# Kernel optimization log

Hardware: AMD Instinct MI355X
Metric: run time of the kernel (lower is better)

The kernel has to match this reference:

```python
import jax, jax.numpy as jnp
import numpy as np


def setup_inputs() -> dict:
    key = jax.random.key(0)
    ks = jax.random.split(key, 16)
    B, T, E, H, V = 64, 24, 512, 1024, 32000
    A = H  # attention_dim == hidden_size in original init
    s = 0.02  # init scale
    n = lambda k, shape: (jax.random.normal(k, shape, jnp.float32) * s)
    return {
        "features": jax.random.normal(ks[0], (B, E), jnp.float32),
        "captions": jax.random.randint(ks[1], (B, T), 0, V, dtype=jnp.int32),
        "lengths": jnp.full((B, 1), T + 1, dtype=jnp.int32),
        # learned parameters
        "emb": n(ks[2], (V, E)),
        "We": n(ks[3], (E, A)), "be": jnp.zeros((A,), jnp.float32),
        "Wd": n(ks[4], (H, A)), "bd": jnp.zeros((A,), jnp.float32),
        "va": n(ks[5], (A,)), "ba": jnp.zeros((), jnp.float32),
        "Wih": n(ks[6], (E, H)), "bih": jnp.zeros((H,), jnp.float32),
        "Wic": n(ks[7], (E, H)), "bic": jnp.zeros((H,), jnp.float32),
        "Wfb": n(ks[8], (H, E)), "bfb": jnp.zeros((E,), jnp.float32),
        "Wi": n(ks[9], (2 * E, 4 * H)), "Wh": n(ks[10], (H, 4 * H)),
        "bl": jnp.zeros((4 * H,), jnp.float32),
        "Wo": n(ks[11], (H, V)), "bo": jnp.zeros((V,), jnp.float32),
    }


def reference(features, captions, lengths, emb, We, be, Wd, bd, va, ba,
              Wih, bih, Wic, bic, Wfb, bfb, Wi, Wh, bl, Wo, bo):
    T = captions.shape[1]
    # embeddings = [features ; embed(captions)] -> [B, T+1, E]
    embeds = jnp.concatenate([features[:, None, :], emb[captions]], axis=1)
    mean_e = embeds.mean(axis=1)
    h = mean_e @ Wih + bih  # init_h
    c = mean_e @ Wic + bic  # init_c
    att1 = embeds @ We + be  # encoder projection, precomputed [B, L, A]

    def step(carry, emb_t):
        h, c = carry
        # additive attention over the full encoded sequence
        score = jnp.einsum('bla,a->bl', jax.nn.relu(att1 + (h @ Wd + bd)[:, None, :]), va) + ba
        alpha = jax.nn.softmax(score, axis=1)
        awe = jnp.einsum('bl,ble->be', alpha, embeds)
        gate = jax.nn.sigmoid(h @ Wfb + bfb)
        x = jnp.concatenate([emb_t, gate * awe], axis=-1)  # [B, 2E]
        z = x @ Wi + h @ Wh + bl
        i, f, g, o = jnp.split(z, 4, axis=-1)  # torch LSTM gate order i,f,g,o
        c = jax.nn.sigmoid(f) * c + jax.nn.sigmoid(i) * jnp.tanh(g)
        h = jax.nn.sigmoid(o) * jnp.tanh(c)
        return (h, c), h @ Wo + bo

    emb_seq = jnp.swapaxes(embeds[:, :T, :], 0, 1)  # [T, B, E]
    (_, _), logits = jax.lax.scan(step, (h, c), emb_seq)
    return jnp.swapaxes(logits, 0, 1)  # [B, T, V]
```

## Files before the change

### kernel.cpp

```cpp
#include <hip/hip_runtime.h>
#include <cstdio>
#include <cstdint>

#define B_ 64
#define T_ 24
#define L_ 25
#define E_ 512
#define H_ 1024
#define A_ 1024
#define V_ 32000
#define HCAT 5632

typedef unsigned short u16;
typedef short bf16x8 __attribute__((ext_vector_type(8)));
typedef float f32x4 __attribute__((ext_vector_type(4)));

__device__ __forceinline__ u16 f2bf(float f) {
    union { float f; unsigned int u; } v; v.f = f;
    unsigned int u = v.u;
    unsigned int r = (u + 0x7FFFu + ((u >> 16) & 1u)) >> 16;
    return (u16)r;
}
__device__ __forceinline__ float bf2f(u16 h) {
    union { unsigned int u; float f; } v; v.u = ((unsigned int)h) << 16;
    return v.f;
}
__device__ __forceinline__ void splitbf(float a, u16& hi, u16& lo) {
    hi = f2bf(a);
    lo = f2bf(a - bf2f(hi));
}
__device__ __forceinline__ float sigf(float x) { return 1.f / (1.f + __expf(-x)); }


__global__ void build_embeds(const float* __restrict__ features, const int* __restrict__ captions,
                             const float* __restrict__ emb, float* __restrict__ embeds,
                             float* __restrict__ mean_eT, u16* __restrict__ embsL2,
                             u16* __restrict__ embsA2) {
    int b = blockIdx.x; int e = threadIdx.x;
    float s = 0.f;
    for (int l = 0; l < L_; ++l) {
        float w;
        if (l == 0) w = features[b * E_ + e];
        else {
            int cap = captions[b * T_ + (l - 1)];
            w = emb[(size_t)cap * E_ + e];
        }
        embeds[(size_t)(b * L_ + l) * E_ + e] = w;
        s += w;
        u16 hi, lo; splitbf(w, hi, lo);
        size_t rl = (size_t)(b * L_ + l) * 1536;
        embsL2[rl + e] = hi; embsL2[rl + 512 + e] = lo; embsL2[rl + 1024 + e] = hi;
        if (l < T_) {
            size_t ra = (size_t)(l * 64 + b) * 1536;
            embsA2[ra + e] = hi; embsA2[ra + 512 + e] = lo; embsA2[ra + 1024 + e] = hi;
        }
    }
    mean_eT[e * B_ + b] = s * (1.f / 25.f);
}

__global__ void transpose_wo(const float* __restrict__ Wo, u16* __restrict__ WoT) {
    __shared__ float tile[32][33];
    int n0 = blockIdx.x * 32, k0 = blockIdx.y * 32;
    int tid = threadIdx.x;
    int tx = tid & 31, ty = tid >> 5;
    for (int i = ty; i < 32; i += 8)
        tile[i][tx] = Wo[(size_t)(k0 + i) * V_ + n0 + tx];
    __syncthreads();
    for (int i = ty; i < 32; i += 8)
        WoT[(size_t)(n0 + i) * H_ + k0 + tx] = f2bf(tile[tx][i]);
}

__global__ void tsplit(const float* __restrict__ W, u16* __restrict__ dst, int K, int srcld) {
    __shared__ float tile[32][33];
    int n0 = blockIdx.x * 32, k0 = blockIdx.y * 32;
    int tid = threadIdx.x;
    int tx = tid & 31, ty = tid >> 5;
    for (int i = ty; i < 32; i += 8)
        tile[i][tx] = W[(size_t)(k0 + i) * srcld + n0 + tx];
    __syncthreads();
    for (int i = ty; i < 32; i += 8) {
        float v = tile[tx][i];
        u16 hi, lo; splitbf(v, hi, lo);
        u16* d = dst + (size_t)(n0 + i) * (3 * K) + (k0 + tx);
        d[0] = hi; d[K] = hi; d[2 * K] = lo;
    }
}

__global__ void build_bcat(const float* __restrict__ bd, const float* __restrict__ bfb,
                           float* __restrict__ bcat) {
    int i = blockIdx.x * 256 + threadIdx.x;
    if (i < HCAT) bcat[i] = (i < 1024) ? bd[i] : ((i < 1536) ? bfb[i - 1024] : 0.f);
}

__global__ __launch_bounds__(1024) void init_hc(const float* __restrict__ mean_eT,
                                                const float* __restrict__ Wih, const float* __restrict__ bih,
                                                const float* __restrict__ Wic, const float* __restrict__ bic,
                                                u16* __restrict__ h2, float* __restrict__ c) {
    int tid = threadIdx.x; int ny = tid & 15, r = tid >> 4;
    int col = blockIdx.x * 16 + ny;
    int cc = (col < H_) ? col : col - H_;
    const float* Wp = (col < H_) ? Wih : Wic;
    const float* bp = (col < H_) ? bih : bic;
    float acc = bp[cc];
    for (int k = 0; k < E_; ++k) acc += mean_eT[k * B_ + r] * Wp[(size_t)k * H_ + cc];
    if (col < H_) {
        u16 hi, lo; splitbf(acc, hi, lo);
        h2[(size_t)r * 3072 + cc] = hi;
        h2[(size_t)r * 3072 + 1024 + cc] = lo;
        h2[(size_t)r * 3072 + 2048 + cc] = hi;
    } else c[r * H_ + cc] = acc;
}

template<int BM, int BN>
__global__ __launch_bounds__(256) void gemm_split(const u16* __restrict__ A2, const u16* __restrict__ B2T,
                                                  const float* __restrict__ bias, float* __restrict__ C,
                                                  int K3, int ldc) {
    constexpr int LDS = 40;
    __shared__ u16 As[BM * LDS];
    __shared__ u16 Bs[BN * LDS];
    constexpr int FM = BM / 32, FN = BN / 32;
    constexpr int ACH = BM / 64, BCH = BN / 64;
    int m0 = blockIdx.x * BM, n0 = blockIdx.y * BN;
    int tid = threadIdx.x, lane = tid & 63, wid = tid >> 6;
    int wm = wid >> 1, wn = wid & 1;

    f32x4 acc[FM][FN];
#pragma unroll
    for (int m = 0; m < FM; ++m)
#pragma unroll
        for (int n = 0; n < FN; ++n) acc[m][n] = (f32x4){0.f, 0.f, 0.f, 0.f};

    const u16* agp[ACH]; u16* asw[ACH];
    const u16* bgp[BCH]; u16* bsw[BCH];
#pragma unroll
    for (int i = 0; i < ACH; ++i) {
        int id = i * 256 + tid; int row = id >> 2, q = id & 3;
        agp[i] = A2 + (size_t)(m0 + row) * K3 + q * 8;
        asw[i] = As + row * LDS + q * 8;
    }
#pragma unroll
    for (int i = 0; i < BCH; ++i) {
        int id = i * 256 + tid; int row = id >> 2, q = id & 3;
        bgp[i] = B2T + (size_t)(n0 + row) * K3 + q * 8;
        bsw[i] = Bs + row * LDS + q * 8;
    }
    int rsel = lane & 15, kg = (lane >> 4) * 8;
    const u16* ard[FM]; const u16* brd[FN];
#pragma unroll
    for (int m = 0; m < FM; ++m) ard[m] = As + (wm * (BM / 2) + m * 16 + rsel) * LDS + kg;
#pragma unroll
    for (int n = 0; n < FN; ++n) brd[n] = Bs + (wn * (BN / 2) + n * 16 + rsel) * LDS + kg;

    uint4 ar[ACH], br[BCH];
#pragma unroll
    for (int i = 0; i < ACH; ++i) ar[i] = *(const uint4*)(agp[i]);
#pragma unroll
    for (int i = 0; i < BCH; ++i) br[i] = *(const uint4*)(bgp[i]);

    int nk = K3 / 32;
    for (int k = 0; k < nk; ++k) {
#pragma unroll
        for (int i = 0; i < ACH; ++i) *(uint4*)(asw[i]) = ar[i];
#pragma unroll
        for (int i = 0; i < BCH; ++i) *(uint4*)(bsw[i]) = br[i];
        __syncthreads();
        if (k + 1 < nk) {
            int kt = (k + 1) * 32;
#pragma unroll
            for (int i = 0; i < ACH; ++i) ar[i] = *(const uint4*)(agp[i] + kt);
#pragma unroll
            for (int i = 0; i < BCH; ++i) br[i] = *(const uint4*)(bgp[i] + kt);
        }
        bf16x8 aF[FM], bF[FN];
#pragma unroll
        for (int m = 0; m < FM; ++m) aF[m] = *(const bf16x8*)(ard[m]);
#pragma unroll
        for (int n = 0; n < FN; ++n) bF[n] = *(const bf16x8*)(brd[n]);
#pragma unroll
        for (int m = 0; m < FM; ++m)
#pragma unroll
            for (int n = 0; n < FN; ++n)
                acc[m][n] = __builtin_amdgcn_mfma_f32_16x16x32_bf16(aF[m], bF[n], acc[m][n], 0, 0, 0);
        __syncthreads();
    }

    int r4 = (lane >> 4) * 4, cn = lane & 15;
#pragma unroll
    for (int n = 0; n < FN; ++n) {
        int gcol = n0 + wn * (BN / 2) + n * 16 + cn;
        float bv = bias[gcol];
#pragma unroll
        for (int m = 0; m < FM; ++m) {
            int gr = m0 + wm * (BM / 2) + m * 16 + r4;
#pragma unroll
            for (int reg = 0; reg < 4; ++reg)
                C[(size_t)(gr + reg) * ldc + gcol] = acc[m][n][reg] + bv;
        }
    }
}


__global__ __launch_bounds__(256) void step_attn(const float* __restrict__ hcat, const float* __restrict__ att1,
                                                 const float* __restrict__ embeds, const float* __restrict__ va,
                                                 u16* __restrict__ x2s) {
    __shared__ float proj_s[1024], va_s[1024], sc_s[32], al_s[32];
    int b = blockIdx.x; int tid = threadIdx.x; int lane = tid & 63; int w = tid >> 6;
    for (int i = tid; i < 1024; i += 256) { proj_s[i] = hcat[b * HCAT + i]; va_s[i] = va[i]; }
    __syncthreads();
    for (int l = w; l < L_; l += 4) {
        const float* arow = att1 + (size_t)(b * L_ + l) * A_;
        float p = 0.f;
        for (int a = lane; a < A_; a += 64) {
            float v = arow[a] + proj_s[a];
            p += fmaxf(v, 0.f) * va_s[a];
        }
        for (int off = 32; off; off >>= 1) p += __shfl_down(p, off);
        if (lane == 0) sc_s[l] = p;
    }
    __syncthreads();
    if (w == 0) {
        float s = (lane < L_) ? sc_s[lane] : -1e30f;
        float m = s;
        for (int off = 32; off; off >>= 1) m = fmaxf(m, __shfl_xor(m, off));
        float e = (lane < L_) ? __expf(s - m) : 0.f;
        float sum = e;
        for (int off = 32; off; off >>= 1) sum += __shfl_xor(sum, off);
        if (lane < L_) al_s[lane] = e / sum;
    }
    __syncthreads();
    for (int e = tid; e < E_; e += 256) {
        float aw = 0.f;
        for (int l = 0; l < L_; ++l) aw += al_s[l] * embeds[(size_t)(b * L_ + l) * E_ + e];
        float gp = hcat[b * HCAT + 1024 + e];
        float v = sigf(gp) * aw;
        u16 hi, lo; splitbf(v, hi, lo);
        x2s[(size_t)b * 1536 + e] = hi;
        x2s[(size_t)b * 1536 + 512 + e] = lo;
        x2s[(size_t)b * 1536 + 1024 + e] = hi;
    }
}

__global__ __launch_bounds__(256) void step_zlstm(const u16* __restrict__ x2s, const u16* __restrict__ WiT2b,
                                                  const float* __restrict__ P1, const float* __restrict__ hcat,
                                                  float* __restrict__ c, u16* __restrict__ h2,
                                                  u16* __restrict__ hs_bf, int t) {
    constexpr int LDS = 40;
    __shared__ u16 As[64 * LDS];
    __shared__ u16 Bs[64 * LDS];
    __shared__ float zb[4][64][16];
    int n0 = blockIdx.x * 16;
    int tid = threadIdx.x, lane = tid & 63, g = tid >> 6;
    f32x4 acc[4];
#pragma unroll
    for (int m = 0; m < 4; ++m) acc[m] = (f32x4){0.f, 0.f, 0.f, 0.f};

    int srow = tid >> 2, sq = tid & 3;
    const u16* agp = x2s + (size_t)srow * 1536 + sq * 8;
    const u16* bgp = WiT2b + (size_t)((srow >> 4) * 1024 + n0 + (srow & 15)) * 1536 + sq * 8;
    u16* asw = As + srow * LDS + sq * 8;
    u16* bsw = Bs + srow * LDS + sq * 8;
    int rsel = lane & 15, kg = (lane >> 4) * 8;

    uint4 ar = *(const uint4*)(agp);
    uint4 br = *(const uint4*)(bgp);
    const int nk = 1536 / 32;
    for (int k = 0; k < nk; ++k) {
        *(uint4*)asw = ar; *(uint4*)bsw = br;
        __syncthreads();
        if (k + 1 < nk) {
            int kt = (k + 1) * 32;
            ar = *(const uint4*)(agp + kt);
            br = *(const uint4*)(bgp + kt);
        }
        bf16x8 bF = *(const bf16x8*)(Bs + (g * 16 + rsel) * LDS + kg);
#pragma unroll
        for (int m = 0; m < 4; ++m) {
            bf16x8 aF = *(const bf16x8*)(As + (m * 16 + rsel) * LDS + kg);
            acc[m] = __builtin_amdgcn_mfma_f32_16x16x32_bf16(aF, bF, acc[m], 0, 0, 0);
        }
        __syncthreads();
    }

    int r4 = (lane >> 4) * 4, cn = lane & 15;
#pragma unroll
    for (int m = 0; m < 4; ++m)
#pragma unroll
        for (int reg = 0; reg < 4; ++reg) {
            int b = m * 16 + r4 + reg;
            int nn = n0 + cn;
            float zv = acc[m][reg] + P1[(size_t)(t * 64 + b) * 4096 + g * 1024 + nn]
                     + hcat[b * HCAT + 1536 + g * 1024 + nn];
            zb[g][b][cn] = zv;
        }
    __syncthreads();
    for (int i = tid; i < 1024; i += 256) {
        int b = i >> 4, cc = i & 15; int nn = n0 + cc;
        float zi = zb[0][b][cc], zf = zb[1][b][cc], zg = zb[2][b][cc], zo = zb[3][b][cc];
        float cold = c[b * H_ + nn];
        float cnew = sigf(zf) * cold + sigf(zi) * tanhf(zg);
        float hh = sigf(zo) * tanhf(cnew);
        c[b * H_ + nn] = cnew;
        u16 hi, lo; splitbf(hh, hi, lo);
        h2[(size_t)b * 3072 + nn] = hi;
        h2[(size_t)b * 3072 + 1024 + nn] = lo;
        h2[(size_t)b * 3072 + 2048 + nn] = hi;
        hs_bf[(size_t)(t * 64 + b) * 1024 + nn] = f2bf(hh);
    }
}

#define BMG 128
#define BNG 128
#define LDSS 40

__global__ __launch_bounds__(256) void gemm_logits(const u16* __restrict__ Abf, const u16* __restrict__ Bbf,
                                                   const float* __restrict__ bo, float* __restrict__ out) {
    __shared__ u16 As[BMG * LDSS];
    __shared__ u16 Bs[BNG * LDSS];
    int m0 = blockIdx.x * BMG;
    int n0 = blockIdx.y * BNG;
    int tid = threadIdx.x; int lane = tid & 63; int wid = tid >> 6;
    int wm = wid >> 1, wn = wid & 1;

    f32x4 acc[4][4];
#pragma unroll
    for (int m = 0; m < 4; ++m)
#pragma unroll
        for (int n = 0; n < 4; ++n) acc[m][n] = (f32x4){0.f, 0.f, 0.f, 0.f};

    int srow = tid >> 1;
    int shalf = tid & 1;
    const u16* ag = Abf + (size_t)(m0 + srow) * H_ + shalf * 16;
    const u16* bg = Bbf + (size_t)(n0 + srow) * H_ + shalf * 16;
    u16* asw = As + srow * LDSS + shalf * 16;
    u16* bsw = Bs + srow * LDSS + shalf * 16;

    int rsel = (lane & 15);
    int kg = (lane >> 4) * 8;

    uint4 a0 = *(const uint4*)(ag), a1 = *(const uint4*)(ag + 8);
    uint4 b0 = *(const uint4*)(bg), b1 = *(const uint4*)(bg + 8);

    for (int kt = 0; kt < H_; kt += 32) {
        *(uint4*)(asw) = a0; *(uint4*)(asw + 8) = a1;
        *(uint4*)(bsw) = b0; *(uint4*)(bsw + 8) = b1;
        __syncthreads();
        if (kt + 32 < H_) {
            a0 = *(const uint4*)(ag + kt + 32); a1 = *(const uint4*)(ag + kt + 40);
            b0 = *(const uint4*)(bg + kt + 32); b1 = *(const uint4*)(bg + kt + 40);
        }
        bf16x8 aF[4], bF[4];
#pragma unroll
        for (int m = 0; m < 4; ++m)
            aF[m] = *(const bf16x8*)(As + (wm * 64 + m * 16 + rsel) * LDSS + kg);
#pragma unroll
        for (int n = 0; n < 4; ++n)
            bF[n] = *(const bf16x8*)(Bs + (wn * 64 + n * 16 + rsel) * LDSS + kg);
#pragma unroll
        for (int m = 0; m < 4; ++m)
#pragma unroll
            for (int n = 0; n < 4; ++n)
                acc[m][n] = __builtin_amdgcn_mfma_f32_16x16x32_bf16(aF[m], bF[n], acc[m][n], 0, 0, 0);
        __syncthreads();
    }

    int r4 = (lane >> 4) * 4;
    int cn = lane & 15;
#pragma unroll
    for (int n = 0; n < 4; ++n) {
        int gn = n0 + wn * 64 + n * 16 + cn;
        float bv = bo[gn];
#pragma unroll
        for (int m = 0; m < 4; ++m) {
            int gmb = m0 + wm * 64 + m * 16 + r4;
#pragma unroll
            for (int reg = 0; reg < 4; ++reg) {
                int gm = gmb + reg;
                int b = gm & 63, t = gm >> 6;
                out[(size_t)(b * T_ + t) * V_ + gn] = acc[m][n][reg] + bv;
            }
        }
    }
}

extern "C" void kernel_launch(void* const* d_in, const int* in_sizes, int n_in,
                              void* d_out, int out_size, void* d_ws, size_t ws_size,
                              hipStream_t stream) {
    const float* features = (const float*)d_in[0];
    const int*   captions = (const int*)d_in[1];
    const float* emb = (const float*)d_in[3];
    const float* We  = (const float*)d_in[4];
    const float* be  = (const float*)d_in[5];
    const float* Wd  = (const float*)d_in[6];
    const float* bd  = (const float*)d_in[7];
    const float* va  = (const float*)d_in[8];
    const float* Wih = (const float*)d_in[10];
    const float* bih = (const float*)d_in[11];
    const float* Wic = (const float*)d_in[12];
    const float* bic = (const float*)d_in[13];
    const float* Wfb = (const float*)d_in[14];
    const float* bfb = (const float*)d_in[15];
    const float* Wi  = (const float*)d_in[16];
    const float* Wh  = (const float*)d_in[17];
    const float* bl  = (const float*)d_in[18];
    const float* Wo  = (const float*)d_in[19];
    const float* bo  = (const float*)d_in[20];
    float* out = (float*)d_out;

    char* ws = (char*)d_ws; size_t wo = 0;
    auto walloc = [&](size_t bytes) -> void* {
        void* p = ws + wo; wo += (bytes + 255) & ~(size_t)255; return p;
    };
    float* embeds  = (float*)walloc((size_t)B_ * L_ * E_ * 4);
    float* mean_eT = (float*)walloc((size_t)E_ * B_ * 4);
    u16*   embsL2  = (u16*)walloc((size_t)B_ * L_ * 1536 * 2);
    u16*   embsA2  = (u16*)walloc((size_t)T_ * B_ * 1536 * 2);
    float* bcat    = (float*)walloc((size_t)HCAT * 4);
    u16*   h2      = (u16*)walloc((size_t)B_ * 3072 * 2);
    float* c       = (float*)walloc((size_t)B_ * H_ * 4);
    float* hcat    = (float*)walloc((size_t)B_ * HCAT * 4);
    u16*   x2s     = (u16*)walloc((size_t)B_ * 1536 * 2);
    u16*   hs_bf   = (u16*)walloc((size_t)T_ * B_ * H_ * 2);
    u16*   WoT     = (u16*)walloc((size_t)V_ * H_ * 2);
    if (wo > ws_size) {
        fprintf(stderr, "kernel_launch: ws too small: need %zu have %zu\n", wo, ws_size);
        return;
    }

    char* ob = (char*)d_out; size_t oo = 0;
    auto oalloc = [&](size_t bytes) -> void* {
        void* p = ob + oo; oo += (bytes + 255) & ~(size_t)255; return p;
    };
    float* P1     = (float*)oalloc((size_t)T_ * B_ * 4096 * 4);
    u16*   WcatT2 = (u16*)oalloc((size_t)HCAT * 3072 * 2);
    u16*   WiT2a  = (u16*)oalloc((size_t)4096 * 1536 * 2);
    u16*   WiT2b  = (u16*)oalloc((size_t)4096 * 1536 * 2);
    u16*   WeT2   = (u16*)oalloc((size_t)1024 * 1536 * 2);
    float* att1   = (float*)oalloc((size_t)B_ * L_ * A_ * 4);

    build_embeds<<<B_, E_, 0, stream>>>(features, captions, emb, embeds, mean_eT, embsL2, embsA2);
    transpose_wo<<<dim3(V_ / 32, H_ / 32), 256, 0, stream>>>(Wo, WoT);
    tsplit<<<dim3(1024 / 32, 1024 / 32), 256, 0, stream>>>(Wd, WcatT2, 1024, 1024);
    tsplit<<<dim3(512 / 32, 1024 / 32), 256, 0, stream>>>(Wfb, WcatT2 + (size_t)1024 * 3072, 1024, 512);
    tsplit<<<dim3(4096 / 32, 1024 / 32), 256, 0, stream>>>(Wh, WcatT2 + (size_t)1536 * 3072, 1024, 4096);
    tsplit<<<dim3(4096 / 32, 512 / 32), 256, 0, stream>>>(Wi, WiT2a, 512, 4096);
    tsplit<<<dim3(4096 / 32, 512 / 32), 256, 0, stream>>>(Wi + (size_t)512 * 4096, WiT2b, 512, 4096);
    tsplit<<<dim3(1024 / 32, 512 / 32), 256, 0, stream>>>(We, WeT2, 512, 1024);
    build_bcat<<<(HCAT + 255) / 256, 256, 0, stream>>>(bd, bfb, bcat);
    init_hc<<<2 * H_ / 16, 1024, 0, stream>>>(mean_eT, Wih, bih, Wic, bic, h2, c);
    gemm_split<64, 64><<<dim3(1600 / 64, 1024 / 64), 256, 0, stream>>>(embsL2, WeT2, be, att1, 1536, 1024);
    gemm_split<128, 64><<<dim3(1536 / 128, 4096 / 64), 256, 0, stream>>>(embsA2, WiT2a, bl, P1, 1536, 4096);

    for (int t = 0; t < T_; ++t) {
        gemm_split<64, 64><<<dim3(1, HCAT / 64), 256, 0, stream>>>(h2, WcatT2, bcat, hcat, 3072, HCAT);
        step_attn<<<B_, 256, 0, stream>>>(hcat, att1, embeds, va, x2s);
        step_zlstm<<<H_ / 16, 256, 0, stream>>>(x2s, WiT2b, P1, hcat, c, h2, hs_bf, t);
    }

    gemm_logits<<<dim3((T_ * B_) / BMG, V_ / BNG), 256, 0, stream>>>(hs_bf, WoT, bo, out);
}
```

Baseline: 2.737 ms.

## Split-K recurrent GEMMs into partial buffers and remap logits workgroups

The per-step h-projection GEMM (88 blocks) and the x·Wi GEMM fused with the LSTM update are replaced by a split-K GEMM that writes partial sums into scratch buffers. The partials plus biases are reduced inside step_attn and a new elementwise step_lstm kernel. This gives each step many more workgroups on a latency-bound recurrence, at the cost of extra partial-sum memory traffic and one more launch per step. The logits GEMM also uses a swizzled 1-D workgroup index to improve cache locality of the weight tiles.

Measured after the change: 2.576 ms. -5.9%, faster.

```diff
diff --git a/kernel.cpp b/kernel.cpp
--- a/kernel.cpp
+++ b/kernel.cpp
@@ -84,12 +84,6 @@
         u16* d = dst + (size_t)(n0 + i) * (3 * K) + (k0 + tx);
         d[0] = hi; d[K] = hi; d[2 * K] = lo;
     }
-}
-
-__global__ void build_bcat(const float* __restrict__ bd, const float* __restrict__ bfb,
-                           float* __restrict__ bcat) {
-    int i = blockIdx.x * 256 + threadIdx.x;
-    if (i < HCAT) bcat[i] = (i < 1024) ? bd[i] : ((i < 1536) ? bfb[i - 1024] : 0.f);
 }
 
 __global__ __launch_bounds__(1024) void init_hc(const float* __restrict__ mean_eT,
@@ -199,13 +193,103 @@
     }
 }
 
-
-__global__ __launch_bounds__(256) void step_attn(const float* __restrict__ hcat, const float* __restrict__ att1,
+template<int KITERS>
+__global__ __launch_bounds__(256, 2) void gemm_sk(const u16* __restrict__ A2, const u16* __restrict__ B2T,
+                                                  float* __restrict__ part, int K3, int N) {
+    constexpr int BK = 128;
+    constexpr int LDS = BK + 8;
+    __shared__ u16 As[64 * LDS];
+    __shared__ u16 Bs[64 * LDS];
+    int n0 = blockIdx.x * 64;
+    int ky = blockIdx.y;
+    int k0 = ky * (BK * KITERS);
+    int tid = threadIdx.x, lane = tid & 63, wid = tid >> 6;
+    int wm = wid >> 1, wn = wid & 1;
+
+    f32x4 acc[2][2];
+#pragma unroll
+    for (int m = 0; m < 2; ++m)
+#pragma unroll
+        for (int n = 0; n < 2; ++n) acc[m][n] = (f32x4){0.f, 0.f, 0.f, 0.f};
+
+    int srow = tid >> 4, scq = tid & 15;
+    const u16* agp[4]; u16* asw[4];
+    const u16* bgp[4]; u16* bsw[4];
+#pragma unroll
+    for (int i = 0; i < 4; ++i) {
+        int row = srow + i * 16;
+        agp[i] = A2 + (size_t)row * K3 + k0 + scq * 8;
+        asw[i] = As + row * LDS + scq * 8;
+        bgp[i] = B2T + (size_t)(n0 + row) * K3 + k0 + scq * 8;
+        bsw[i] = Bs + row * LDS + scq * 8;
+    }
+    int rsel = lane & 15, kg = (lane >> 4) * 8;
+    const u16* ard[2]; const u16* brd[2];
+#pragma unroll
+    for (int m = 0; m < 2; ++m) ard[m] = As + (wm * 32 + m * 16 + rsel) * LDS + kg;
+#pragma unroll
+    for (int n = 0; n < 2; ++n) brd[n] = Bs + (wn * 32 + n * 16 + rsel) * LDS + kg;
+
+    uint4 ar[4], br[4];
+#pragma unroll
+    for (int i = 0; i < 4; ++i) { ar[i] = *(const uint4*)(agp[i]); br[i] = *(const uint4*)(bgp[i]); }
+
+    for (int it = 0; it < KITERS; ++it) {
+#pragma unroll
+        for (int i = 0; i < 4; ++i) { *(uint4*)(asw[i]) = ar[i]; *(uint4*)(bsw[i]) = br[i]; }
+        __syncthreads();
+        if (it + 1 < KITERS) {
+            int kt = (it + 1) * BK;
+#pragma unroll
+            for (int i = 0; i < 4; ++i) {
+                ar[i] = *(const uint4*)(agp[i] + kt);
+                br[i] = *(const uint4*)(bgp[i] + kt);
+            }
+        }
+#pragma unroll
+        for (int kk = 0; kk < BK / 32; ++kk) {
+            bf16x8 aF[2], bF[2];
+#pragma unroll
+            for (int m = 0; m < 2; ++m) aF[m] = *(const bf16x8*)(ard[m] + kk * 32);
+#pragma unroll
+            for (int n = 0; n < 2; ++n) bF[n] = *(const bf16x8*)(brd[n] + kk * 32);
+#pragma unroll
+            for (int m = 0; m < 2; ++m)
+#pragma unroll
+                for (int n = 0; n < 2; ++n)
+                    acc[m][n] = __builtin_amdgcn_mfma_f32_16x16x32_bf16(aF[m], bF[n], acc[m][n], 0, 0, 0);
+        }
+        __syncthreads();
+    }
+
+    float* p = part + (size_t)ky * 64 * N;
+    int r4 = (lane >> 4) * 4, cn = lane & 15;
+#pragma unroll
+    for (int n = 0; n < 2; ++n) {
+        int gcol = n0 + wn * 32 + n * 16 + cn;
+#pragma unroll
+        for (int m = 0; m < 2; ++m) {
+            int gr = wm * 32 + m * 16 + r4;
+#pragma unroll
+            for (int reg = 0; reg < 4; ++reg)
+                p[(size_t)(gr + reg) * N + gcol] = acc[m][n][reg];
+        }
+    }
+}
+
+
+__global__ __launch_bounds__(256) void step_attn(const float* __restrict__ hpart, const float* __restrict__ att1,
                                                  const float* __restrict__ embeds, const float* __restrict__ va,
+                                                 const float* __restrict__ bd, const float* __restrict__ bfb,
                                                  u16* __restrict__ x2s) {
     __shared__ float proj_s[1024], va_s[1024], sc_s[32], al_s[32];
     int b = blockIdx.x; int tid = threadIdx.x; int lane = tid & 63; int w = tid >> 6;
-    for (int i = tid; i < 1024; i += 256) { proj_s[i] = hcat[b * HCAT + i]; va_s[i] = va[i]; }
+    for (int i = tid; i < 1024; i += 256) {
+        float s = bd[i];
+#pragma unroll
+        for (int ky = 0; ky < 6; ++ky) s += hpart[(size_t)ky * 64 * HCAT + b * HCAT + i];
+        proj_s[i] = s; va_s[i] = va[i];
+    }
     __syncthreads();
     for (int l = w; l < L_; l += 4) {
         const float* arow = att1 + (size_t)(b * L_ + l) * A_;
@@ -231,7 +315,9 @@
     for (int e = tid; e < E_; e += 256) {
         float aw = 0.f;
         for (int l = 0; l < L_; ++l) aw += al_s[l] * embeds[(size_t)(b * L_ + l) * E_ + e];
-        float gp = hcat[b * HCAT + 1024 + e];
+        float gp = bfb[e];
+#pragma unroll
+        for (int ky = 0; ky < 6; ++ky) gp += hpart[(size_t)ky * 64 * HCAT + b * HCAT + 1024 + e];
         float v = sigf(gp) * aw;
         u16 hi, lo; splitbf(v, hi, lo);
         x2s[(size_t)b * 1536 + e] = hi;
@@ -240,84 +326,48 @@
     }
 }
 
-__global__ __launch_bounds__(256) void step_zlstm(const u16* __restrict__ x2s, const u16* __restrict__ WiT2b,
-                                                  const float* __restrict__ P1, const float* __restrict__ hcat,
-                                                  float* __restrict__ c, u16* __restrict__ h2,
-                                                  u16* __restrict__ hs_bf, int t) {
-    constexpr int LDS = 40;
-    __shared__ u16 As[64 * LDS];
-    __shared__ u16 Bs[64 * LDS];
-    __shared__ float zb[4][64][16];
-    int n0 = blockIdx.x * 16;
-    int tid = threadIdx.x, lane = tid & 63, g = tid >> 6;
-    f32x4 acc[4];
-#pragma unroll
-    for (int m = 0; m < 4; ++m) acc[m] = (f32x4){0.f, 0.f, 0.f, 0.f};
-
-    int srow = tid >> 2, sq = tid & 3;
-    const u16* agp = x2s + (size_t)srow * 1536 + sq * 8;
-    const u16* bgp = WiT2b + (size_t)((srow >> 4) * 1024 + n0 + (srow & 15)) * 1536 + sq * 8;
-    u16* asw = As + srow * LDS + sq * 8;
-    u16* bsw = Bs + srow * LDS + sq * 8;
-    int rsel = lane & 15, kg = (lane >> 4) * 8;
-
-    uint4 ar = *(const uint4*)(agp);
-    uint4 br = *(const uint4*)(bgp);
-    const int nk = 1536 / 32;
-    for (int k = 0; k < nk; ++k) {
-        *(uint4*)asw = ar; *(uint4*)bsw = br;
-        __syncthreads();
-        if (k + 1 < nk) {
-            int kt = (k + 1) * 32;
-            ar = *(const uint4*)(agp + kt);
-            br = *(const uint4*)(bgp + kt);
-        }
-        bf16x8 bF = *(const bf16x8*)(Bs + (g * 16 + rsel) * LDS + kg);
-#pragma unroll
-        for (int m = 0; m < 4; ++m) {
-            bf16x8 aF = *(const bf16x8*)(As + (m * 16 + rsel) * LDS + kg);
-            acc[m] = __builtin_amdgcn_mfma_f32_16x16x32_bf16(aF, bF, acc[m], 0, 0, 0);
-        }
-        __syncthreads();
-    }
-
-    int r4 = (lane >> 4) * 4, cn = lane & 15;
-#pragma unroll
-    for (int m = 0; m < 4; ++m)
-#pragma unroll
-        for (int reg = 0; reg < 4; ++reg) {
-            int b = m * 16 + r4 + reg;
-            int nn = n0 + cn;
-            float zv = acc[m][reg] + P1[(size_t)(t * 64 + b) * 4096 + g * 1024 + nn]
-                     + hcat[b * HCAT + 1536 + g * 1024 + nn];
-            zb[g][b][cn] = zv;
-        }
-    __syncthreads();
-    for (int i = tid; i < 1024; i += 256) {
-        int b = i >> 4, cc = i & 15; int nn = n0 + cc;
-        float zi = zb[0][b][cc], zf = zb[1][b][cc], zg = zb[2][b][cc], zo = zb[3][b][cc];
-        float cold = c[b * H_ + nn];
-        float cnew = sigf(zf) * cold + sigf(zi) * tanhf(zg);
-        float hh = sigf(zo) * tanhf(cnew);
-        c[b * H_ + nn] = cnew;
-        u16 hi, lo; splitbf(hh, hi, lo);
-        h2[(size_t)b * 3072 + nn] = hi;
-        h2[(size_t)b * 3072 + 1024 + nn] = lo;
-        h2[(size_t)b * 3072 + 2048 + nn] = hi;
-        hs_bf[(size_t)(t * 64 + b) * 1024 + nn] = f2bf(hh);
-    }
+__global__ __launch_bounds__(256) void step_lstm(const float* __restrict__ zpart, const float* __restrict__ P1,
+                                                 const float* __restrict__ hpart, float* __restrict__ c,
+                                                 u16* __restrict__ h2, u16* __restrict__ hs_bf, int t) {
+    int idx = blockIdx.x * 256 + threadIdx.x;
+    int b = idx >> 10, n = idx & 1023;
+    float zv[4];
+#pragma unroll
+    for (int g = 0; g < 4; ++g) {
+        int col = g * 1024 + n;
+        float s = P1[(size_t)(t * 64 + b) * 4096 + col];
+#pragma unroll
+        for (int ky = 0; ky < 3; ++ky) s += zpart[(size_t)ky * 64 * 4096 + b * 4096 + col];
+#pragma unroll
+        for (int ky = 0; ky < 6; ++ky) s += hpart[(size_t)ky * 64 * HCAT + b * HCAT + 1536 + col];
+        zv[g] = s;
+    }
+    float cold = c[b * H_ + n];
+    float cnew = sigf(zv[1]) * cold + sigf(zv[0]) * tanhf(zv[2]);
+    float hh = sigf(zv[3]) * tanhf(cnew);
+    c[b * H_ + n] = cnew;
+    u16 hi, lo; splitbf(hh, hi, lo);
+    h2[(size_t)b * 3072 + n] = hi;
+    h2[(size_t)b * 3072 + 1024 + n] = lo;
+    h2[(size_t)b * 3072 + 2048 + n] = hi;
+    hs_bf[(size_t)(t * 64 + b) * 1024 + n] = f2bf(hh);
 }
 
 #define BMG 128
 #define BNG 128
 #define LDSS 40
+#define NWG_M (T_ * B_ / BMG)
+#define NWG_N (V_ / BNG)
+#define NWG (NWG_M * NWG_N)
 
 __global__ __launch_bounds__(256) void gemm_logits(const u16* __restrict__ Abf, const u16* __restrict__ Bbf,
                                                    const float* __restrict__ bo, float* __restrict__ out) {
     __shared__ u16 As[BMG * LDSS];
     __shared__ u16 Bs[BNG * LDSS];
-    int m0 = blockIdx.x * BMG;
-    int n0 = blockIdx.y * BNG;
+    int lid = blockIdx.x;
+    int wg = (lid & 7) * (NWG / 8) + (lid >> 3);
+    int m0 = (wg % NWG_M) * BMG;
+    int n0 = (wg / NWG_M) * BNG;
     int tid = threadIdx.x; int lane = tid & 63; int wid = tid >> 6;
     int wm = wid >> 1, wn = wid & 1;
 
@@ -414,13 +464,13 @@
     float* mean_eT = (float*)walloc((size_t)E_ * B_ * 4);
     u16*   embsL2  = (u16*)walloc((size_t)B_ * L_ * 1536 * 2);
     u16*   embsA2  = (u16*)walloc((size_t)T_ * B_ * 1536 * 2);
-    float* bcat    = (float*)walloc((size_t)HCAT * 4);
     u16*   h2      = (u16*)walloc((size_t)B_ * 3072 * 2);
     float* c       = (float*)walloc((size_t)B_ * H_ * 4);
-    float* hcat    = (float*)walloc((size_t)B_ * HCAT * 4);
     u16*   x2s     = (u16*)walloc((size_t)B_ * 1536 * 2);
     u16*   hs_bf   = (u16*)walloc((size_t)T_ * B_ * H_ * 2);
     u16*   WoT     = (u16*)walloc((size_t)V_ * H_ * 2);
+    float* hpart   = (float*)walloc((size_t)6 * B_ * HCAT * 4);
+    float* zpart   = (float*)walloc((size_t)3 * B_ * 4096 * 4);
     if (wo > ws_size) {
         fprintf(stderr, "kernel_launch: ws too small: need %zu have %zu\n", wo, ws_size);
         return;
@@ -445,16 +495,16 @@
     tsplit<<<dim3(4096 / 32, 512 / 32), 256, 0, stream>>>(Wi, WiT2a, 512, 4096);
     tsplit<<<dim3(4096 / 32, 512 / 32), 256, 0, stream>>>(Wi + (size_t)512 * 4096, WiT2b, 512, 4096);
     tsplit<<<dim3(1024 / 32, 512 / 32), 256, 0, stream>>>(We, WeT2, 512, 1024);
-    build_bcat<<<(HCAT + 255) / 256, 256, 0, stream>>>(bd, bfb, bcat);
     init_hc<<<2 * H_ / 16, 1024, 0, stream>>>(mean_eT, Wih, bih, Wic, bic, h2, c);
     gemm_split<64, 64><<<dim3(1600 / 64, 1024 / 64), 256, 0, stream>>>(embsL2, WeT2, be, att1, 1536, 1024);
     gemm_split<128, 64><<<dim3(1536 / 128, 4096 / 64), 256, 0, stream>>>(embsA2, WiT2a, bl, P1, 1536, 4096);
 
     for (int t = 0; t < T_; ++t) {
-        gemm_split<64, 64><<<dim3(1, HCAT / 64), 256, 0, stream>>>(h2, WcatT2, bcat, hcat, 3072, HCAT);
-        step_attn<<<B_, 256, 0, stream>>>(hcat, att1, embeds, va, x2s);
-        step_zlstm<<<H_ / 16, 256, 0, stream>>>(x2s, WiT2b, P1, hcat, c, h2, hs_bf, t);
-    }
-
-    gemm_logits<<<dim3((T_ * B_) / BMG, V_ / BNG), 256, 0, stream>>>(hs_bf, WoT, bo, out);
-}
+        gemm_sk<4><<<dim3(HCAT / 64, 6), 256, 0, stream>>>(h2, WcatT2, hpart, 3072, HCAT);
+        step_attn<<<B_, 256, 0, stream>>>(hpart, att1, embeds, va, bd, bfb, x2s);
+        gemm_sk<4><<<dim3(4096 / 64, 3), 256, 0, stream>>>(x2s, WiT2b, zpart, 1536, 4096);
+        step_lstm<<<B_ * H_ / 256, 256, 0, stream>>>(zpart, P1, hpart, c, h2, hs_bf, t);
+    }
+
+    gemm_logits<<<NWG, 256, 0, stream>>>(hs_bf, WoT, bo, out);
+}
```
